# Optimization experiments

Hardware: AMD Instinct MI355X
Metric: run time of the kernel (lower is better)

The kernel has to match this reference:

```python
import jax, jax.numpy as jnp
import numpy as np

B, S, D_IN, D_FF, D_OUT, E = 4, 2048, 1024, 4096, 1024, 8


def setup_inputs() -> dict:
    key = jax.random.key(0)
    ks = jax.random.split(key, 8)
    s = lambda k, shape, fan: jax.random.normal(k, shape, dtype=jnp.float32) * (1.0 / np.sqrt(fan))
    return {
        "x": jax.random.normal(ks[0], (B, S, D_IN), dtype=jnp.float32),
        "switch_w": s(ks[1], (D_IN, E), D_IN),
        "switch_b": jnp.zeros((E,), dtype=jnp.float32),
        "w1": s(ks[2], (E, D_IN, D_FF), D_IN),
        "b1": jnp.zeros((E, D_FF), dtype=jnp.float32),
        "w2": s(ks[3], (E, D_FF, D_OUT), D_FF),
        "b2": jnp.zeros((E, D_OUT), dtype=jnp.float32),
    }


def reference(x, switch_w, switch_b, w1, b1, w2, b2):
    b, s, d = x.shape
    n_experts = w1.shape[0]
    xf = x.reshape(-1, d)                                   # [T, d]
    route_prob = jax.nn.softmax(xf @ switch_w + switch_b, axis=-1)  # [T, E]
    route_prob_max = jnp.max(route_prob, axis=-1)           # [T]
    routes = jnp.argmax(route_prob, axis=-1)                # [T] int, constant wrt grads

    # Per-expert FFN applied to all tokens, combined with top-1 one-hot mask
    # (drop_tokens=False -> every token goes to exactly its argmax expert).
    h = jax.nn.relu(jnp.einsum('td,edf->etf', xf, w1) + b1[:, None, :])   # [E, T, f]
    y_all = jnp.einsum('etf,efo->eto', h, w2) + b2[:, None, :]            # [E, T, d_out]
    onehot = jax.nn.one_hot(routes, n_experts, dtype=xf.dtype)            # [T, E]
    y = jnp.einsum('eto,te->to', y_all, onehot)             # dispatch-combine

    # is_scale_prob=True: scale output by routing probability
    y = y * route_prob_max[:, None]

    counts = onehot.sum(axis=0)                             # tokens per expert
    route_frac = counts / counts.sum()
    aux_loss = n_experts * jnp.sum(route_frac * route_prob.sum(axis=0))

    return y.reshape(b, s, -1), aux_loss
```

## Files before the change

kernel.cpp:

```cpp
#include <hip/hip_runtime.h>
#include <cstdint>
#include <cstddef>

#define NT   8192
#define DIN  1024
#define DFF  4096
#define DOUT 1024
#define NEXP 8

typedef float  f32x4v __attribute__((ext_vector_type(4)));
typedef short  s16x8  __attribute__((ext_vector_type(8)));
typedef short  s16x4  __attribute__((ext_vector_type(4)));

__device__ __forceinline__ ushort f2bf(float f) {
  union { float f; uint32_t u; } c; c.f = f;
  uint32_t u = c.u;
  return (ushort)((u + 0x7fffu + ((u >> 16) & 1u)) >> 16);
}

__global__ __launch_bounds__(256) void router_kernel(
    const float* __restrict__ x, const float* __restrict__ sw,
    const float* __restrict__ sb,
    int* __restrict__ routes, int* __restrict__ posArr,
    float* __restrict__ pmaxArr,
    int* __restrict__ cnt, float* __restrict__ probsum) {
  __shared__ int   sRoute[64];
  __shared__ float sProb[4][NEXP];
  __shared__ int   sBase[NEXP];

  const int lane = threadIdx.x & 63;
  const int w    = threadIdx.x >> 6;
  const int t0   = blockIdx.x * 64;

  float bias[NEXP];
#pragma unroll
  for (int e = 0; e < NEXP; e++) bias[e] = sb[e];

  float wprob[NEXP];
#pragma unroll
  for (int e = 0; e < NEXP; e++) wprob[e] = 0.0f;

  for (int k = 0; k < 16; k++) {
    const int t = t0 + w * 16 + k;
    const float* xr = x + (size_t)t * DIN;
    float acc[NEXP];
#pragma unroll
    for (int e = 0; e < NEXP; e++) acc[e] = 0.0f;
#pragma unroll
    for (int it = 0; it < DIN / 64; it++) {
      const int i = it * 64 + lane;
      const float xv = xr[i];
      const float4 s0 = *(const float4*)(sw + (size_t)i * NEXP);
      const float4 s1 = *(const float4*)(sw + (size_t)i * NEXP + 4);
      acc[0] += xv * s0.x; acc[1] += xv * s0.y; acc[2] += xv * s0.z; acc[3] += xv * s0.w;
      acc[4] += xv * s1.x; acc[5] += xv * s1.y; acc[6] += xv * s1.z; acc[7] += xv * s1.w;
    }
#pragma unroll
    for (int e = 0; e < NEXP; e++) {
#pragma unroll
      for (int off = 32; off > 0; off >>= 1) acc[e] += __shfl_xor(acc[e], off, 64);
    }
    float m = acc[0] + bias[0]; int am = 0;
    float lg[NEXP];
#pragma unroll
    for (int e = 0; e < NEXP; e++) {
      lg[e] = acc[e] + bias[e];
      if (lg[e] > m) { m = lg[e]; am = e; }
    }
    float esum = 0.0f;
    float pe[NEXP];
#pragma unroll
    for (int e = 0; e < NEXP; e++) { pe[e] = __expf(lg[e] - m); esum += pe[e]; }
    const float inv = 1.0f / esum;
#pragma unroll
    for (int e = 0; e < NEXP; e++) wprob[e] += pe[e] * inv;
    if (lane == 0) {
      routes[t] = am;
      pmaxArr[t] = inv;
      sRoute[w * 16 + k] = am;
    }
  }
  if (lane == 0) {
#pragma unroll
    for (int e = 0; e < NEXP; e++) sProb[w][e] = wprob[e];
  }
  __syncthreads();

  const int tid = threadIdx.x;
  if (tid < NEXP) {
    float s = sProb[0][tid] + sProb[1][tid] + sProb[2][tid] + sProb[3][tid];
    atomicAdd(&probsum[tid], s);
    int c = 0;
#pragma unroll
    for (int j = 0; j < 64; j++) c += (sRoute[j] == tid);
    sBase[tid] = atomicAdd(&cnt[tid], c);
  }
  __syncthreads();

  if (tid < 64) {
    const int r = sRoute[tid];
    int rank = 0;
    for (int j = 0; j < 64; j++) rank += (j < tid) & (sRoute[j] == r);
    posArr[t0 + tid] = sBase[r] + rank;
  }
}

__global__ void offsets_aux_kernel(const int* __restrict__ cnt, const float* __restrict__ probsum,
                                   int* __restrict__ offsets, float* __restrict__ auxout) {
  if (threadIdx.x == 0) {
    int o = 0; float aux = 0.0f;
    for (int e = 0; e < NEXP; e++) {
      offsets[e] = o; o += cnt[e];
      aux += (float)cnt[e] * probsum[e];
    }
    offsets[NEXP] = o;
    auxout[0] = aux * ((float)NEXP / (float)NT);
  }
}

__global__ void gather_kernel(const float* __restrict__ x, const int* __restrict__ routes,
                              const int* __restrict__ posArr, const int* __restrict__ offsets,
                              int* __restrict__ perm, ushort* __restrict__ Xg) {
  const int lane = threadIdx.x & 63;
  const int t = (blockIdx.x * blockDim.x + threadIdx.x) >> 6;
  if (t >= NT) return;
  const int slot = offsets[routes[t]] + posArr[t];
  if (lane == 0) perm[slot] = t;
  const float* src = x + (size_t)t * DIN;
  ushort* dst = Xg + (size_t)slot * DIN;
#pragma unroll
  for (int half = 0; half < 2; half++) {
    int i = half * 512 + lane * 8;
    float4 v0 = *(const float4*)(src + i);
    float4 v1 = *(const float4*)(src + i + 4);
    s16x8 p;
    p[0] = (short)f2bf(v0.x); p[1] = (short)f2bf(v0.y);
    p[2] = (short)f2bf(v0.z); p[3] = (short)f2bf(v0.w);
    p[4] = (short)f2bf(v1.x); p[5] = (short)f2bf(v1.y);
    p[6] = (short)f2bf(v1.z); p[7] = (short)f2bf(v1.w);
    *(s16x8*)(dst + i) = p;
  }
}

__global__ void transpose_cvt_kernel(const float* __restrict__ src, ushort* __restrict__ dst,
                                     const int K, const int N) {
  __shared__ float tile[64][65];
  const int ntn = N >> 6;
  const int ntk = K >> 6;
  int b = blockIdx.x;
  const int tn = b % ntn; b /= ntn;
  const int tk = b % ntk; const int e = b / ntk;
  const float* s = src + ((size_t)e * K + (size_t)tk * 64) * N + (size_t)tn * 64;
  const int c4 = (threadIdx.x & 15) * 4;
  const int r0 = threadIdx.x >> 4;
#pragma unroll
  for (int p = 0; p < 4; p++) {
    const int row = r0 + p * 16;
    float4 v = *(const float4*)(s + (size_t)row * N + c4);
    tile[row][c4 + 0] = v.x; tile[row][c4 + 1] = v.y;
    tile[row][c4 + 2] = v.z; tile[row][c4 + 3] = v.w;
  }
  __syncthreads();
  ushort* d = dst + ((size_t)e * N + (size_t)tn * 64) * K + (size_t)tk * 64;
#pragma unroll
  for (int p = 0; p < 4; p++) {
    const int nrow = r0 + p * 16;
    s16x4 o;
    o[0] = (short)f2bf(tile[c4 + 0][nrow]);
    o[1] = (short)f2bf(tile[c4 + 1][nrow]);
    o[2] = (short)f2bf(tile[c4 + 2][nrow]);
    o[3] = (short)f2bf(tile[c4 + 3][nrow]);
    *(s16x4*)(d + (size_t)nrow * K + c4) = o;
  }
}

#define GLD16(g, l)                                                                        \
  __builtin_amdgcn_global_load_lds((const __attribute__((address_space(1))) uint32_t*)(g), \
                                   (__attribute__((address_space(3))) uint32_t*)(l), 16, 0, 0)

#define SBAR()   asm volatile("s_barrier" ::: "memory")
#define WAITV(n) asm volatile("s_waitcnt vmcnt(" #n ")" ::: "memory")

template <int KDIM, int EPI>
__global__ __launch_bounds__(512, 1) void moe_gemm256_kernel(
    const ushort* __restrict__ A,
    const ushort* __restrict__ BT,
    const float* __restrict__ bias,
    const int* __restrict__ offsets,
    ushort* __restrict__ Hout,
    float* __restrict__ Y,
    const int* __restrict__ perm, const float* __restrict__ pmaxArr,
    const int N) {
  __shared__ ushort sA[4][8192];
  __shared__ ushort sB[4][8192];
  const int e = blockIdx.z;
  const int mlimit = offsets[e + 1];
  const int m0 = offsets[e] + blockIdx.y * 256;
  if (m0 >= mlimit) return;
  const int n0 = blockIdx.x * 256;
  const int tid = threadIdx.x;
  const int lane = tid & 63;
  const int wid = tid >> 6;
  const int wr = wid >> 2;
  const int wc = wid & 3;
  const int rsel = lane & 15;
  const int lhi = lane >> 4;

  const int srow = wid * 8 + (lane >> 3);
  const int scol = ((lane & 7) ^ (lane >> 3)) * 8;
  const ushort* gA = A + (size_t)(m0 + srow) * KDIM + scol;
  const ushort* gB = BT + ((size_t)e * N + n0 + srow) * KDIM + scol;
  const int ldst = tid * 8;

#define STAGE_A(s, h, kt)                                                   \
  do {                                                                      \
    const ushort* g_ = gA + (size_t)((h) * 128) * KDIM + (size_t)(kt) * 64; \
    GLD16(g_, &sA[s][ldst]);                                                \
    GLD16(g_ + (size_t)64 * KDIM, &sA[s][ldst + 4096]);                     \
  } while (0)
#define STAGE_B(s, h, kt)                                                   \
  do {                                                                      \
    const ushort* g_ = gB + (size_t)((h) * 128) * KDIM + (size_t)(kt) * 64; \
    GLD16(g_, &sB[s][ldst]);                                                \
    GLD16(g_ + (size_t)64 * KDIM, &sB[s][ldst + 4096]);                     \
  } while (0)

  f32x4v acc[2][2][4][2];
#pragma unroll
  for (int i = 0; i < 2; i++)
#pragma unroll
    for (int j = 0; j < 2; j++)
#pragma unroll
      for (int mf = 0; mf < 4; mf++)
#pragma unroll
        for (int nf = 0; nf < 2; nf++) acc[i][j][mf][nf] = (f32x4v)0.0f;

  const int rsw = rsel & 7;
  const int sw0 = ((lhi) ^ rsw) * 8;
  const int sw1 = ((4 + lhi) ^ rsw) * 8;
  int arow[4], brow[2];
#pragma unroll
  for (int mf = 0; mf < 4; mf++) arow[mf] = (wr * 64 + mf * 16 + rsel) * 64;
#pragma unroll
  for (int nf = 0; nf < 2; nf++) brow[nf] = (wc * 32 + nf * 16 + rsel) * 64;

  s16x8 a[4][2], b0[2][2], b1[2][2];

#define LDA(slot)                                                      \
  do {                                                                 \
    _Pragma("unroll") for (int mf = 0; mf < 4; mf++) {                 \
      a[mf][0] = *(const s16x8*)&sA[slot][arow[mf] + sw0];             \
      a[mf][1] = *(const s16x8*)&sA[slot][arow[mf] + sw1];             \
    }                                                                  \
  } while (0)
#define LDB(dst, slot)                                                 \
  do {                                                                 \
    _Pragma("unroll") for (int nf = 0; nf < 2; nf++) {                 \
      dst[nf][0] = *(const s16x8*)&sB[slot][brow[nf] + sw0];           \
      dst[nf][1] = *(const s16x8*)&sB[slot][brow[nf] + sw1];           \
    }                                                                  \
  } while (0)
#define MFMAQ(MG, NG, BB)                                              \
  do {                                                                 \
    __builtin_amdgcn_s_setprio(1);                                     \
    _Pragma("unroll") for (int mf = 0; mf < 4; mf++)                   \
    _Pragma("unroll") for (int nf = 0; nf < 2; nf++)                   \
    _Pragma("unroll") for (int ks = 0; ks < 2; ks++)                   \
      acc[MG][NG][mf][nf] = __builtin_amdgcn_mfma_f32_16x16x32_bf16(   \
          a[mf][ks], BB[nf][ks], acc[MG][NG][mf][nf], 0, 0, 0);        \
    __builtin_amdgcn_s_setprio(0);                                     \
  } while (0)

  constexpr int NS = KDIM / 64;
  STAGE_A(0, 0, 0);
  STAGE_B(0, 0, 0);
  STAGE_B(1, 1, 0);
  STAGE_A(1, 1, 0);
  WAITV(4);
  SBAR();

#pragma unroll 2
  for (int t = 0; t < NS; ++t) {
    const int s0 = (2 * t) & 3, s1 = (2 * t + 1) & 3;
    const int sn0 = (2 * t + 2) & 3, sn1 = (2 * t + 3) & 3;
    const bool more = (t + 1 < NS);
    LDA(s0);
    LDB(b0, s0);
    if (more) STAGE_A(sn0, 0, t + 1);
    SBAR();
    MFMAQ(0, 0, b0);
    if (more) { WAITV(4); } else { WAITV(2); }
    SBAR();
    LDB(b1, s1);
    if (more) STAGE_B(sn0, 0, t + 1);
    SBAR();
    MFMAQ(0, 1, b1);
    if (more) { WAITV(4); } else { WAITV(0); }
    SBAR();
    LDA(s1);
    if (more) STAGE_B(sn1, 1, t + 1);
    SBAR();
    MFMAQ(1, 1, b1);
    SBAR();
    if (more) STAGE_A(sn1, 1, t + 1);
    SBAR();
    MFMAQ(1, 0, b0);
    if (more) { WAITV(4); }
    SBAR();
  }
#undef LDA
#undef LDB
#undef MFMAQ
#undef STAGE_A
#undef STAGE_B

  float bv[2][2];
#pragma unroll
  for (int ng = 0; ng < 2; ng++)
#pragma unroll
    for (int nf = 0; nf < 2; nf++)
      bv[ng][nf] = bias[(size_t)e * N + n0 + ng * 128 + wc * 32 + nf * 16 + rsel];
#pragma unroll
  for (int mg = 0; mg < 2; mg++) {
#pragma unroll
    for (int mf = 0; mf < 4; mf++) {
#pragma unroll
      for (int r = 0; r < 4; r++) {
        const int grow = m0 + mg * 128 + wr * 64 + mf * 16 + lhi * 4 + r;
        if (grow < mlimit) {
          if (EPI == 0) {
            ushort* hrow = Hout + (size_t)grow * N + n0;
#pragma unroll
            for (int ng = 0; ng < 2; ng++)
#pragma unroll
              for (int nf = 0; nf < 2; nf++) {
                float v = acc[mg][ng][mf][nf][r] + bv[ng][nf];
                hrow[ng * 128 + wc * 32 + nf * 16 + rsel] = f2bf(fmaxf(v, 0.0f));
              }
          } else {
            const int tok = perm[grow];
            const float sc = pmaxArr[tok];
            float* yrow = Y + (size_t)tok * N + n0;
#pragma unroll
            for (int ng = 0; ng < 2; ng++)
#pragma unroll
              for (int nf = 0; nf < 2; nf++)
                yrow[ng * 128 + wc * 32 + nf * 16 + rsel] =
                    (acc[mg][ng][mf][nf][r] + bv[ng][nf]) * sc;
          }
        }
      }
    }
  }
}

extern "C" void kernel_launch(void* const* d_in, const int* in_sizes, int n_in,
                              void* d_out, int out_size, void* d_ws, size_t ws_size,
                              hipStream_t stream) {
  const float* x  = (const float*)d_in[0];
  const float* sw = (const float*)d_in[1];
  const float* sb = (const float*)d_in[2];
  const float* w1 = (const float*)d_in[3];
  const float* b1 = (const float*)d_in[4];
  const float* w2 = (const float*)d_in[5];
  const float* b2 = (const float*)d_in[6];
  float* out = (float*)d_out;
  float* auxp = out + (size_t)NT * DOUT;

  char* wsb = (char*)d_ws;
  int*   cnt      = (int*)wsb;
  float* probsum  = (float*)(wsb + 32);
  int*   offsets  = (int*)(wsb + 64);
  int*   routes   = (int*)(wsb + 256);
  int*   posArr   = routes + NT;
  float* pmaxArr  = (float*)(posArr + NT);
  int*   perm     = (int*)(pmaxArr + NT);
  ushort* Xg = (ushort*)(wsb + 256 + (size_t)4 * 4 * NT);
  ushort* Hg = Xg + (size_t)(NT + 256) * DIN;
  ushort* Wt = Hg + (size_t)(NT + 256) * DFF;
  size_t needed = (size_t)((char*)Wt - wsb) + (size_t)NEXP * DFF * DIN * 2;
  if (ws_size < needed) return;

  hipMemsetAsync(d_ws, 0, 64, stream);

  router_kernel<<<NT / 64, 256, 0, stream>>>(x, sw, sb, routes, posArr, pmaxArr, cnt, probsum);
  offsets_aux_kernel<<<1, 64, 0, stream>>>(cnt, probsum, offsets, auxp);
  gather_kernel<<<NT / 4, 256, 0, stream>>>(x, routes, posArr, offsets, perm, Xg);

  transpose_cvt_kernel<<<NEXP * (DIN / 64) * (DFF / 64), 256, 0, stream>>>(w1, Wt, DIN, DFF);
  moe_gemm256_kernel<DIN, 0><<<dim3(DFF / 256, 8, NEXP), 512, 0, stream>>>(
      Xg, Wt, b1, offsets, Hg, nullptr, nullptr, nullptr, DFF);

  transpose_cvt_kernel<<<NEXP * (DFF / 64) * (DOUT / 64), 256, 0, stream>>>(w2, Wt, DFF, DOUT);
  moe_gemm256_kernel<DFF, 1><<<dim3(DOUT / 256, 8, NEXP), 512, 0, stream>>>(
      Hg, Wt, b2, offsets, nullptr, out, perm, pmaxArr, DOUT);
}
```

Measured before the change: 356.2 us.

## Use 128-row M tiles for second MoE GEMM and interleave experts in grid

Adds a template parameter that picks the M tile height. The down-projection GEMM now uses 128x256 tiles with a reduced A buffer and its own simplified pipeline, and all launches use a 1D grid that interleaves experts across consecutive block IDs. The down-projection grid has only 4 N-tiles, so the aim is more active blocks and better load balance across CUs when expert token counts are uneven. In exchange, each block reuses A less and the tile has lower arithmetic intensity. The grid of 10 M-blocks per expert may also leave tokens uncovered if an expert receives more than 1280 tokens.

Result: slower. 383.6 us (+7.7%).

```diff
diff --git a/kernel.cpp b/kernel.cpp
--- a/kernel.cpp
+++ b/kernel.cpp
@@ -181,7 +181,7 @@
 #define SBAR()   asm volatile("s_barrier" ::: "memory")
 #define WAITV(n) asm volatile("s_waitcnt vmcnt(" #n ")" ::: "memory")
 
-template <int KDIM, int EPI>
+template <int KDIM, int EPI, int MH>
 __global__ __launch_bounds__(512, 1) void moe_gemm256_kernel(
     const ushort* __restrict__ A,
     const ushort* __restrict__ BT,
@@ -191,13 +191,19 @@
     float* __restrict__ Y,
     const int* __restrict__ perm, const float* __restrict__ pmaxArr,
     const int N) {
-  __shared__ ushort sA[4][8192];
+  constexpr int ASLOTS = (MH == 2) ? 4 : 2;
+  __shared__ ushort sA[ASLOTS][8192];
   __shared__ ushort sB[4][8192];
-  const int e = blockIdx.z;
+  const int fid = blockIdx.x;
+  const int e = fid & 7;
+  const int rem = fid >> 3;
+  const int nxb = N / 256;
+  const int bx = rem % nxb;
+  const int by = rem / nxb;
   const int mlimit = offsets[e + 1];
-  const int m0 = offsets[e] + blockIdx.y * 256;
+  const int m0 = offsets[e] + by * (MH * 128);
   if (m0 >= mlimit) return;
-  const int n0 = blockIdx.x * 256;
+  const int n0 = bx * 256;
   const int tid = threadIdx.x;
   const int lane = tid & 63;
   const int wid = tid >> 6;
@@ -225,9 +231,9 @@
     GLD16(g_ + (size_t)64 * KDIM, &sB[s][ldst + 4096]);                     \
   } while (0)
 
-  f32x4v acc[2][2][4][2];
-#pragma unroll
-  for (int i = 0; i < 2; i++)
+  f32x4v acc[MH][2][4][2];
+#pragma unroll
+  for (int i = 0; i < MH; i++)
 #pragma unroll
     for (int j = 0; j < 2; j++)
 #pragma unroll
@@ -272,41 +278,69 @@
   } while (0)
 
   constexpr int NS = KDIM / 64;
-  STAGE_A(0, 0, 0);
-  STAGE_B(0, 0, 0);
-  STAGE_B(1, 1, 0);
-  STAGE_A(1, 1, 0);
-  WAITV(4);
-  SBAR();
-
+
+  if constexpr (MH == 2) {
+    STAGE_A(0, 0, 0);
+    STAGE_B(0, 0, 0);
+    STAGE_B(1, 1, 0);
+    STAGE_A(1, 1, 0);
+    WAITV(4);
+    SBAR();
 #pragma unroll 2
-  for (int t = 0; t < NS; ++t) {
-    const int s0 = (2 * t) & 3, s1 = (2 * t + 1) & 3;
-    const int sn0 = (2 * t + 2) & 3, sn1 = (2 * t + 3) & 3;
-    const bool more = (t + 1 < NS);
-    LDA(s0);
-    LDB(b0, s0);
-    if (more) STAGE_A(sn0, 0, t + 1);
+    for (int t = 0; t < NS; ++t) {
+      const int s0 = (2 * t) & 3, s1 = (2 * t + 1) & 3;
+      const int sn0 = (2 * t + 2) & 3, sn1 = (2 * t + 3) & 3;
+      const bool more = (t + 1 < NS);
+      LDA(s0);
+      LDB(b0, s0);
+      if (more) STAGE_A(sn0, 0, t + 1);
+      SBAR();
+      MFMAQ(0, 0, b0);
+      if (more) { WAITV(4); } else { WAITV(2); }
+      SBAR();
+      LDB(b1, s1);
+      if (more) STAGE_B(sn0, 0, t + 1);
+      SBAR();
+      MFMAQ(0, 1, b1);
+      if (more) { WAITV(4); } else { WAITV(0); }
+      SBAR();
+      LDA(s1);
+      if (more) STAGE_B(sn1, 1, t + 1);
+      SBAR();
+      MFMAQ(1, 1, b1);
+      SBAR();
+      if (more) STAGE_A(sn1, 1, t + 1);
+      SBAR();
+      MFMAQ(1, 0, b0);
+      if (more) { WAITV(4); }
+      SBAR();
+    }
+  } else {
+    STAGE_A(0, 0, 0);
+    STAGE_B(0, 0, 0);
+    STAGE_B(1, 1, 0);
+    WAITV(0);
     SBAR();
-    MFMAQ(0, 0, b0);
-    if (more) { WAITV(4); } else { WAITV(2); }
-    SBAR();
-    LDB(b1, s1);
-    if (more) STAGE_B(sn0, 0, t + 1);
-    SBAR();
-    MFMAQ(0, 1, b1);
-    if (more) { WAITV(4); } else { WAITV(0); }
-    SBAR();
-    LDA(s1);
-    if (more) STAGE_B(sn1, 1, t + 1);
-    SBAR();
-    MFMAQ(1, 1, b1);
-    SBAR();
-    if (more) STAGE_A(sn1, 1, t + 1);
-    SBAR();
-    MFMAQ(1, 0, b0);
-    if (more) { WAITV(4); }
-    SBAR();
+#pragma unroll 2
+    for (int t = 0; t < NS; ++t) {
+      const int as = t & 1, asn = (t + 1) & 1;
+      const int bs0 = (2 * t) & 3, bs1 = (2 * t + 1) & 3;
+      const int bsn0 = (2 * t + 2) & 3, bsn1 = (2 * t + 3) & 3;
+      const bool more = (t + 1 < NS);
+      LDA(as);
+      LDB(b0, bs0);
+      if (more) { STAGE_A(asn, 0, t + 1); STAGE_B(bsn0, 0, t + 1); }
+      SBAR();
+      MFMAQ(0, 0, b0);
+      if (more) { WAITV(4); } else { WAITV(0); }
+      SBAR();
+      LDB(b1, bs1);
+      if (more) STAGE_B(bsn1, 1, t + 1);
+      SBAR();
+      MFMAQ(0, 1, b1);
+      if (more) { WAITV(2); }
+      SBAR();
+    }
   }
 #undef LDA
 #undef LDB
@@ -321,7 +355,7 @@
     for (int nf = 0; nf < 2; nf++)
       bv[ng][nf] = bias[(size_t)e * N + n0 + ng * 128 + wc * 32 + nf * 16 + rsel];
 #pragma unroll
-  for (int mg = 0; mg < 2; mg++) {
+  for (int mg = 0; mg < MH; mg++) {
 #pragma unroll
     for (int mf = 0; mf < 4; mf++) {
 #pragma unroll
@@ -388,10 +422,10 @@
   gather_kernel<<<NT / 4, 256, 0, stream>>>(x, routes, posArr, offsets, perm, Xg);
 
   transpose_cvt_kernel<<<NEXP * (DIN / 64) * (DFF / 64), 256, 0, stream>>>(w1, Wt, DIN, DFF);
-  moe_gemm256_kernel<DIN, 0><<<dim3(DFF / 256, 8, NEXP), 512, 0, stream>>>(
+  moe_gemm256_kernel<DIN, 0, 2><<<8 * (DFF / 256) * 8, 512, 0, stream>>>(
       Xg, Wt, b1, offsets, Hg, nullptr, nullptr, nullptr, DFF);
 
   transpose_cvt_kernel<<<NEXP * (DFF / 64) * (DOUT / 64), 256, 0, stream>>>(w2, Wt, DFF, DOUT);
-  moe_gemm256_kernel<DFF, 1><<<dim3(DOUT / 256, 8, NEXP), 512, 0, stream>>>(
+  moe_gemm256_kernel<DFF, 1, 1><<<8 * (DOUT / 256) * 10, 512, 0, stream>>>(
       Hg, Wt, b2, offsets, nullptr, out, perm, pmaxArr, DOUT);
 }
```
